# Kernel tuning notes

Measured on AMD Instinct MI355X. Metric: run time of the kernel, lower is better.

## Reference

```python
import jax, jax.numpy as jnp
import numpy as np

B, S, E, H, V = 64, 400, 512, 512, 32000


def setup_inputs() -> dict:
    key = jax.random.key(0)
    ks = jax.random.split(key, 16)
    sc = lambda fan: 1.0 / np.sqrt(fan)
    u = lambda k, shape, fan: jax.random.uniform(k, shape, jnp.float32, -sc(fan), sc(fan))
    mask = jax.random.randint(ks[3], (B, S), 0, 2).astype(bool)
    mask = mask.at[:, 0].set(True)  # ensure at least one valid position per row
    return {
        "decoder_input": jax.random.normal(ks[0], (B, E), jnp.float32),
        "previous_hidden_state": jax.random.normal(ks[1], (B, H), jnp.float32),
        "encoder_output": jax.random.normal(ks[2], (B, S, 2 * H), jnp.float32),
        "mask": mask,
        # GRUCell params (torch layout: weight_ih [3H,E], weight_hh [3H,H])
        "w_ih": u(ks[4], (3 * H, E), H),
        "w_hh": u(ks[5], (3 * H, H), H),
        "b_ih": u(ks[6], (3 * H,), H),
        "b_hh": u(ks[7], (3 * H,), H),
        # Attention params
        "Wh_w": u(ks[8], (H, 2 * H), 2 * H),
        "Wh_b": u(ks[9], (H,), 2 * H),
        "Ws_w": u(ks[10], (H, H), H),
        "Ws_b": u(ks[11], (H,), H),
        "vatt_w": u(ks[12], (1, H), H),  # Linear(H,1,bias=False)
        # Output projections
        "V_w": u(ks[13], (H, 3 * H), 3 * H),
        "V_b": u(ks[13], (H,), 3 * H),
        "Vhat_w": u(ks[14], (V, H), H),
        "Vhat_b": u(ks[15], (V,), H),
    }


def reference(decoder_input, previous_hidden_state, encoder_output, mask,
              w_ih, w_hh, b_ih, b_hh, Wh_w, Wh_b, Ws_w, Ws_b, vatt_w,
              V_w, V_b, Vhat_w, Vhat_b):
    # --- GRUCell step (torch semantics) ---
    gi = decoder_input @ w_ih.T + b_ih                  # [B, 3H]
    gh = previous_hidden_state @ w_hh.T + b_hh          # [B, 3H]
    i_r, i_z, i_n = jnp.split(gi, 3, axis=-1)
    h_r, h_z, h_n = jnp.split(gh, 3, axis=-1)
    r = jax.nn.sigmoid(i_r + h_r)
    z = jax.nn.sigmoid(i_z + h_z)
    n = jnp.tanh(i_n + r * h_n)
    hidden = (1.0 - z) * n + z * previous_hidden_state  # [B, H]

    # --- Additive (Bahdanau) attention ---
    feat = jnp.tanh(encoder_output @ Wh_w.T + Wh_b
                    + (hidden @ Ws_w.T + Ws_b)[:, None, :])   # [B, S, H]
    scores = jnp.einsum('bsh,h->bs', feat, vatt_w[0])          # [B, S]
    scores = jnp.where(mask, scores, -jnp.inf)
    attn_dist = jax.nn.softmax(scores, axis=-1)                # [B, S]

    # --- Context + output projection ---
    context_vector = jnp.einsum('bs,bsd->bd', attn_dist, encoder_output)  # [B, 2H]
    out = jnp.concatenate([hidden, context_vector], axis=-1) @ V_w.T + V_b  # [B, H]
    logits = out @ Vhat_w.T + Vhat_b                                        # [B, V]
    vocab_dist = jax.nn.softmax(logits, axis=-1)
    return (vocab_dist, attn_dist, context_vector, hidden)
```

## Files before the change

### kernel.cpp

```cpp
#include <hip/hip_runtime.h>
#include <hip/hip_bf16.h>
#include <stdint.h>

#define DI __device__ __forceinline__

using f32x2 = __attribute__((ext_vector_type(2))) float;
using f32x4 = __attribute__((ext_vector_type(4))) float;
using s16x8 = __attribute__((ext_vector_type(8))) short;

#define BB 64
#define SS 400
#define HH 512
#define VVOC 32000
#define MTOT (BB*SS)

DI short bf16r(float f){
  __hip_bfloat16 h = __float2bfloat16(f);
  union { __hip_bfloat16 h; short s; } u; u.h = h; return u.s;
}
DI float sigm(float x){ return 1.f/(1.f + __expf(-x)); }
DI float tanhfast(float x){ x = fminf(x, 12.f); float e = __expf(2.f*x); return (e-1.f)/(e+1.f); }

DI void gload16b(const __hip_bfloat16* g, short* l){
  __builtin_amdgcn_global_load_lds(
      (const __attribute__((address_space(1))) __hip_bfloat16*)g,
      (__attribute__((address_space(3))) short*)l, 16, 0, 0);
}

DI float blkmax(float v, float* red, int t){
  #pragma unroll
  for (int o = 32; o; o >>= 1) v = fmaxf(v, __shfl_xor(v, o));
  if ((t & 63) == 0) red[t >> 6] = v;
  __syncthreads();
  v = fmaxf(fmaxf(red[0], red[1]), fmaxf(red[2], red[3]));
  __syncthreads();
  return v;
}
DI float blksum(float v, float* red, int t){
  #pragma unroll
  for (int o = 32; o; o >>= 1) v += __shfl_xor(v, o);
  if ((t & 63) == 0) red[t >> 6] = v;
  __syncthreads();
  v = red[0] + red[1] + red[2] + red[3];
  __syncthreads();
  return v;
}

DI s16x8 cvt8v(f32x4 a, f32x4 b){
  s16x8 o;
  o[0]=bf16r(a[0]); o[1]=bf16r(a[1]); o[2]=bf16r(a[2]); o[3]=bf16r(a[3]);
  o[4]=bf16r(b[0]); o[5]=bf16r(b[1]); o[6]=bf16r(b[2]); o[7]=bf16r(b[3]);
  return o;
}
DI s16x8 cvt8(const float* src){
  return cvt8v(((const f32x4*)src)[0], ((const f32x4*)src)[1]);
}

DI s16x8 fragload16(const short* tile, int rbase, int kk, int l){
  int r = rbase + (l & 15);
  int c = (kk >> 3) + (l >> 4);
  int slot = c ^ (r & 7);
  return *(const s16x8*)(tile + r*64 + slot*8);
}

DI void mfma_small_body(const float* __restrict__ A, const float* __restrict__ W,
                        float* __restrict__ P, int K, int N, int c0, int kseg,
                        short* lsa, short* lsb, int t)
{
  const int kbeg = kseg*64;
  const int l = t & 63, w = t >> 6;
  #pragma unroll
  for (int q = 0; q < 2; ++q) {
    int it = q*256 + t;
    int r = it >> 3, c = it & 7;
    int slot = (c ^ (r & 7)) << 3;
    *(s16x8*)(lsa + r*64 + slot) = cvt8(A + (size_t)r*K + kbeg + c*8);
    *(s16x8*)(lsb + r*64 + slot) = cvt8(W + (size_t)(c0 + r)*K + kbeg + c*8);
  }
  __syncthreads();
  f32x4 acc[4];
  #pragma unroll
  for (int m = 0; m < 4; ++m) { f32x4 z = {0.f,0.f,0.f,0.f}; acc[m] = z; }
  #pragma unroll
  for (int kk = 0; kk < 64; kk += 32) {
    s16x8 bf = fragload16(lsb, w*16, kk, l);
    #pragma unroll
    for (int m = 0; m < 4; ++m) {
      s16x8 af = fragload16(lsa, m*16, kk, l);
      acc[m] = __builtin_amdgcn_mfma_f32_16x16x32_bf16(af, bf, acc[m], 0, 0, 0);
    }
  }
  const int kq = l >> 4, lc = l & 15;
  const int col = c0 + w*16 + lc;
  size_t pbase = (size_t)kseg * 64 * N;
  #pragma unroll
  for (int m = 0; m < 4; ++m)
    #pragma unroll
    for (int j = 0; j < 4; ++j)
      P[pbase + (size_t)(m*16 + kq*4 + j)*N + col] = acc[m][j];
}

__global__ __launch_bounds__(256) void k_pre(
    const float* __restrict__ wh, short* __restrict__ wh16,
    const unsigned int* __restrict__ mask, int mwords, int* __restrict__ flags,
    const float* __restrict__ x, const float* __restrict__ hprev,
    const float* __restrict__ w_ih, const float* __restrict__ w_hh,
    float* __restrict__ GI, float* __restrict__ GH)
{
  __shared__ __align__(16) short ls[2][64*64];
  int b = blockIdx.x, t = threadIdx.x;
  if (b < 256) {
    int i = b*256 + t;
    ((s16x8*)wh16)[i] = cvt8(wh + (size_t)i*8);
  } else if (b < 264) {
    __shared__ int f;
    if (t == 0) f = 0;
    __syncthreads();
    int loc = 0;
    for (int i = (b-256)*256 + t; i < mwords; i += 8*256) loc |= (mask[i] > 1u) ? 1 : 0;
    if (loc) atomicOr(&f, 1);
    __syncthreads();
    if (t == 0) flags[b-256] = f;
  } else {
    int gb = b - 264;
    int colI = gb % 24;
    int kseg = (gb / 24) % 8;
    int z    = gb / 192;
    mfma_small_body(z ? hprev : x, z ? w_hh : w_ih, z ? GH : GI,
                    512, 1536, colI*64, kseg, ls[0], ls[1], t);
  }
}

__global__ void gru_gate(const float* __restrict__ GI, const float* __restrict__ GH,
                         const float* __restrict__ b_ih, const float* __restrict__ b_hh,
                         const float* __restrict__ hprev, float* __restrict__ hid,
                         float* __restrict__ concat)
{
  int i = blockIdx.x*256 + threadIdx.x;
  int b = i >> 9, h = i & 511;
  float ir=0, iz=0, inn=0, hr=0, hz=0, hn=0;
  #pragma unroll
  for (int s = 0; s < 8; ++s) {
    const float* gi = GI + (size_t)s*(64*1536) + b*1536;
    const float* gh = GH + (size_t)s*(64*1536) + b*1536;
    ir += gi[h];      iz += gi[512+h];  inn += gi[1024+h];
    hr += gh[h];      hz += gh[512+h];  hn  += gh[1024+h];
  }
  ir += b_ih[h]; iz += b_ih[512+h]; inn += b_ih[1024+h];
  hr += b_hh[h]; hz += b_hh[512+h]; hn  += b_hh[1024+h];
  float r = sigm(ir + hr), z = sigm(iz + hz);
  float n = tanhfast(inn + r*hn);
  float hv = (1.f - z)*n + z*hprev[i];
  hid[i] = hv;
  concat[b*1536 + h] = hv;
}

__global__ __launch_bounds__(256) void mfma_small(
    const float* __restrict__ A, const float* __restrict__ W,
    float* __restrict__ P, int K, int N)
{
  __shared__ __align__(16) short ls[2][64*64];
  mfma_small_body(A, W, P, K, N, blockIdx.x*64, blockIdx.y, ls[0], ls[1], threadIdx.x);
}

__global__ void combineN(const float* __restrict__ P, const float* __restrict__ b1,
                         const float* __restrict__ b2, float* __restrict__ dstv,
                         int N, int total, int nseg)
{
  int i = blockIdx.x*256 + threadIdx.x;
  if (i >= total) return;
  float a = 0.f;
  for (int s = 0; s < nseg; ++s) a += P[(size_t)s*total + i];
  int c = i % N;
  if (b1) a += b1[c];
  if (b2) a += b2[c];
  dstv[i] = a;
}

__global__ __launch_bounds__(512, 2) void score_gemm_bf16(
    const float* __restrict__ A, const __hip_bfloat16* __restrict__ Bw,
    const float* __restrict__ qv, const float* __restrict__ vb, float* __restrict__ dst)
{
  __shared__ __align__(16) short lsa[128*64];
  __shared__ __align__(16) short lsb[2][512*64];
  const int t = threadIdx.x;
  const int l = t & 63;
  const int w = t >> 6;
  const int wm = w >> 2;
  const int wn = w & 3;
  const int phys = blockIdx.x;
  const int logical = (phys & 7)*25 + (phys >> 3);
  const int mrow = logical * 128;

  f32x4 par[2][2];
  #define A_LOAD(k0)                                                              \
    _Pragma("unroll")                                                             \
    for (int q = 0; q < 2; ++q) {                                                 \
      int ci = q*512 + t; int r = ci >> 3, c = ci & 7;                            \
      const f32x4* ap = (const f32x4*)(A + (size_t)(mrow + r)*1024 + (k0) + c*8); \
      par[q][0] = ap[0]; par[q][1] = ap[1];                                       \
    }
  #define A_WRITE()                                                               \
    _Pragma("unroll")                                                             \
    for (int q = 0; q < 2; ++q) {                                                 \
      int ci = q*512 + t; int r = ci >> 3, c = ci & 7;                            \
      *(s16x8*)(lsa + r*64 + ((c ^ (r & 7)) << 3)) = cvt8v(par[q][0], par[q][1]); \
    }
  #define B_STAGE(buf, k0)                                                        \
    _Pragma("unroll")                                                             \
    for (int i = 0; i < 8; ++i) {                                                 \
      int ci = i*512 + t; int r = ci >> 3, slot = ci & 7;                         \
      int c = slot ^ (r & 7);                                                     \
      gload16b(Bw + (size_t)r*1024 + (k0) + c*8, lsb[buf] + ci*8);                \
    }

  f32x4 acc[4][8];
  #pragma unroll
  for (int m = 0; m < 4; ++m)
    #pragma unroll
    for (int n = 0; n < 8; ++n) { f32x4 z = {0.f,0.f,0.f,0.f}; acc[m][n] = z; }

  A_LOAD(0)
  A_WRITE()
  B_STAGE(0, 0)
  __syncthreads();

  int cur = 0;
  for (int k = 0; k < 16; ++k) {
    if (k < 15) {
      A_LOAD((k+1)*64)
      B_STAGE(cur ^ 1, (k+1)*64)
    }
    #pragma unroll
    for (int kk = 0; kk < 64; kk += 32) {
      s16x8 bf[8];
      #pragma unroll
      for (int n = 0; n < 8; ++n) bf[n] = fragload16(lsb[cur], wn*128 + n*16, kk, l);
      #pragma unroll
      for (int m = 0; m < 4; ++m) {
        s16x8 af = fragload16(lsa, wm*64 + m*16, kk, l);
        #pragma unroll
        for (int n = 0; n < 8; ++n)
          acc[m][n] = __builtin_amdgcn_mfma_f32_16x16x32_bf16(af, bf[n], acc[m][n], 0, 0, 0);
      }
    }
    __syncthreads();
    if (k < 15) A_WRITE()
    __syncthreads();
    cur ^= 1;
  }
  #undef A_LOAD
  #undef A_WRITE
  #undef B_STAGE

  const int kq = l >> 4, lc = l & 15;
  float vv[8];
  #pragma unroll
  for (int n = 0; n < 8; ++n) vv[n] = vb[wn*128 + n*16 + lc];
  float* red = (float*)lsa;
  #pragma unroll
  for (int m = 0; m < 4; ++m) {
    #pragma unroll
    for (int j = 0; j < 4; ++j) {
      int rl = wm*64 + m*16 + kq*4 + j;
      int r = mrow + rl;
      int b = r / SS;
      const float* qb = qv + b*HH + wn*128 + lc;
      float ps = 0.f;
      #pragma unroll
      for (int n = 0; n < 8; ++n) ps += vv[n]*tanhfast(acc[m][n][j] + qb[n*16]);
      #pragma unroll
      for (int o = 1; o < 16; o <<= 1) ps += __shfl_xor(ps, o);
      if (lc == 0) red[rl*4 + wn] = ps;
    }
  }
  __syncthreads();
  if (t < 128) {
    float s = red[t*4] + red[t*4+1] + red[t*4+2] + red[t*4+3];
    dst[mrow + t] = s;
  }
}

__global__ __launch_bounds__(256) void vocab_gemm(
    const float* __restrict__ OUTm, const float* __restrict__ Vhat,
    const float* __restrict__ Vb, float* __restrict__ logits,
    float* __restrict__ MAXP, float* __restrict__ SUMP)
{
  __shared__ __align__(16) short lsa[64*64];
  __shared__ __align__(16) short lsb[64*64];
  __shared__ float red[64][8];
  const int t = threadIdx.x, l = t & 63, w = t >> 6;
  const int vrow0 = blockIdx.x * 64;

  f32x4 acc[4];
  #pragma unroll
  for (int m = 0; m < 4; ++m) { f32x4 z = {0.f,0.f,0.f,0.f}; acc[m] = z; }

  f32x4 pa0[2][2], pb0[2][2], pa1[2][2], pb1[2][2];

  #define VLOAD(pa, pb, k0)                                                     \
    _Pragma("unroll")                                                           \
    for (int q = 0; q < 2; ++q) {                                               \
      int it = q*256 + t; int r = it >> 3, c = it & 7;                          \
      const f32x4* ap = (const f32x4*)(OUTm + (size_t)r*512 + (k0) + c*8);      \
      pa[q][0] = ap[0]; pa[q][1] = ap[1];                                       \
      const f32x4* bp = (const f32x4*)(Vhat + (size_t)(vrow0 + r)*512 + (k0) + c*8); \
      pb[q][0] = bp[0]; pb[q][1] = bp[1];                                       \
    }
  #define VSTEP(pa, pb)                                                         \
    _Pragma("unroll")                                                           \
    for (int q = 0; q < 2; ++q) {                                               \
      int it = q*256 + t; int r = it >> 3, c = it & 7;                          \
      int slot = (c ^ (r & 7)) << 3;                                            \
      *(s16x8*)(lsa + r*64 + slot) = cvt8v(pa[q][0], pa[q][1]);                 \
      *(s16x8*)(lsb + r*64 + slot) = cvt8v(pb[q][0], pb[q][1]);                 \
    }                                                                           \
    __syncthreads();                                                            \
    _Pragma("unroll")                                                           \
    for (int kk = 0; kk < 64; kk += 32) {                                       \
      s16x8 bf = fragload16(lsb, w*16, kk, l);                                  \
      _Pragma("unroll")                                                         \
      for (int m = 0; m < 4; ++m) {                                             \
        s16x8 af = fragload16(lsa, m*16, kk, l);                                \
        acc[m] = __builtin_amdgcn_mfma_f32_16x16x32_bf16(af, bf, acc[m], 0,0,0);\
      }                                                                         \
    }                                                                           \
    __syncthreads();

  VLOAD(pa0, pb0, 0)
  #pragma unroll
  for (int s2 = 0; s2 < 4; ++s2) {
    int k0 = s2*128;
    if (k0 + 64 < 512) { VLOAD(pa1, pb1, k0 + 64) }
    VSTEP(pa0, pb0)
    if (k0 + 128 < 512) { VLOAD(pa0, pb0, k0 + 128) }
    VSTEP(pa1, pb1)
  }
  #undef VLOAD
  #undef VSTEP

  const int kq = l >> 4, lc = l & 15;
  const int voc = vrow0 + w*16 + lc;
  const float bias = Vb[voc];
  #pragma unroll
  for (int m = 0; m < 4; ++m)
    #pragma unroll
    for (int j = 0; j < 4; ++j) {
      acc[m][j] += bias;
      logits[(size_t)(m*16 + kq*4 + j)*VVOC + voc] = acc[m][j];
    }
  #pragma unroll
  for (int m = 0; m < 4; ++m)
    #pragma unroll
    for (int j = 0; j < 4; ++j) {
      float v = acc[m][j];
      #pragma unroll
      for (int o = 1; o < 16; o <<= 1) v = fmaxf(v, __shfl_xor(v, o));
      if (lc == 0) red[m*16 + kq*4 + j][w] = v;
    }
  __syncthreads();
  float gmax[4][4];
  #pragma unroll
  for (int m = 0; m < 4; ++m)
    #pragma unroll
    for (int j = 0; j < 4; ++j) {
      int row = m*16 + kq*4 + j;
      gmax[m][j] = fmaxf(fmaxf(red[row][0], red[row][1]), fmaxf(red[row][2], red[row][3]));
    }
  __syncthreads();
  #pragma unroll
  for (int m = 0; m < 4; ++m)
    #pragma unroll
    for (int j = 0; j < 4; ++j) {
      float s = __expf(acc[m][j] - gmax[m][j]);
      #pragma unroll
      for (int o = 1; o < 16; o <<= 1) s += __shfl_xor(s, o);
      if (lc == 0) red[m*16 + kq*4 + j][4 + w] = s;
    }
  __syncthreads();
  if (t < 64) {
    float M = fmaxf(fmaxf(red[t][0], red[t][1]), fmaxf(red[t][2], red[t][3]));
    float S = red[t][4] + red[t][5] + red[t][6] + red[t][7];
    MAXP[blockIdx.x*64 + t] = M;
    SUMP[blockIdx.x*64 + t] = S;
  }
}

__global__ __launch_bounds__(256) void vnorm(
    const float* __restrict__ MAXP, const float* __restrict__ SUMP,
    float* __restrict__ logits)
{
  __shared__ float red[4];
  int b = blockIdx.x, q = blockIdx.y, t = threadIdx.x;
  float m = -INFINITY;
  for (int i = t; i < 500; i += 256) m = fmaxf(m, MAXP[i*64 + b]);
  m = blkmax(m, red, t);
  float z = 0.f;
  for (int i = t; i < 500; i += 256) z += SUMP[i*64 + b] * __expf(MAXP[i*64 + b] - m);
  z = blksum(z, red, t);
  float inv = 1.f / z;
  f32x4* p = (f32x4*)(logits + (size_t)b*VVOC + q*8000);
  for (int i = t; i < 2000; i += 256) {
    f32x4 v = p[i];
    #pragma unroll
    for (int c = 0; c < 4; ++c) v[c] = __expf(v[c] - m) * inv;
    p[i] = v;
  }
}

__global__ void softmax_s(const float* __restrict__ score, const void* __restrict__ mask,
                          const int* __restrict__ flags, float* __restrict__ attn)
{
  __shared__ float red[4];
  int b = blockIdx.x, t = threadIdx.x;
  bool isbyte = (flags[0]|flags[1]|flags[2]|flags[3]|flags[4]|flags[5]|flags[6]|flags[7]) != 0;
  float sc0, sc1 = -INFINITY;
  {
    bool mv = isbyte ? (((const unsigned char*)mask)[b*SS + t] != 0)
                     : (((const int*)mask)[b*SS + t] != 0);
    sc0 = mv ? score[b*SS + t] : -INFINITY;
  }
  int s1 = t + 256;
  if (s1 < SS) {
    bool mv = isbyte ? (((const unsigned char*)mask)[b*SS + s1] != 0)
                     : (((const int*)mask)[b*SS + s1] != 0);
    sc1 = mv ? score[b*SS + s1] : -INFINITY;
  }
  float mx = blkmax(fmaxf(sc0, sc1), red, t);
  float e0 = __expf(sc0 - mx), e1 = __expf(sc1 - mx);
  float sum = blksum(e0 + e1, red, t);
  float inv = 1.f / sum;
  attn[b*SS + t] = e0 * inv;
  if (s1 < SS) attn[b*SS + s1] = e1 * inv;
}

__global__ void ctx_part(const float* __restrict__ attn, const float* __restrict__ enc,
                         float* __restrict__ CTXP)
{
  int b = blockIdx.x, dh = blockIdx.y, sq = blockIdx.z;
  int d0 = dh*512 + threadIdx.x*2;
  const float* a = attn + b*SS + sq*50;
  const float* e = enc + (size_t)(b*SS + sq*50)*1024 + d0;
  float lo = 0.f, hi = 0.f;
  #pragma unroll 5
  for (int s = 0; s < 50; ++s) {
    f32x2 u = *(const f32x2*)(e + (size_t)s*1024);
    float av = a[s];
    lo += av * u[0];
    hi += av * u[1];
  }
  float* dst = CTXP + (size_t)sq*65536 + b*1024 + d0;
  dst[0] = lo; dst[1] = hi;
}

__global__ void ctx_combine(const float* __restrict__ CTXP, float* __restrict__ ctx,
                            float* __restrict__ concat)
{
  int b = blockIdx.x;
  for (int d = threadIdx.x; d < 1024; d += 256) {
    float s = 0.f;
    #pragma unroll
    for (int q = 0; q < 8; ++q) s += CTXP[q*65536 + b*1024 + d];
    ctx[b*1024 + d] = s;
    concat[b*1536 + 512 + d] = s;
  }
}

extern "C" void kernel_launch(void* const* d_in, const int* in_sizes, int n_in,
                              void* d_out, int out_size, void* d_ws, size_t ws_size,
                              hipStream_t stream) {
  (void)in_sizes; (void)n_in; (void)out_size; (void)ws_size;
  const float* x      = (const float*)d_in[0];
  const float* hprev  = (const float*)d_in[1];
  const float* enc    = (const float*)d_in[2];
  const void*  mask   = d_in[3];
  const float* w_ih   = (const float*)d_in[4];
  const float* w_hh   = (const float*)d_in[5];
  const float* b_ih   = (const float*)d_in[6];
  const float* b_hh   = (const float*)d_in[7];
  const float* Wh_w   = (const float*)d_in[8];
  const float* Wh_b   = (const float*)d_in[9];
  const float* Ws_w   = (const float*)d_in[10];
  const float* Ws_b   = (const float*)d_in[11];
  const float* vatt   = (const float*)d_in[12];
  const float* V_w    = (const float*)d_in[13];
  const float* V_b    = (const float*)d_in[14];
  const float* Vhat_w = (const float*)d_in[15];
  const float* Vhat_b = (const float*)d_in[16];

  float* out   = (float*)d_out;
  float* vocab = out;
  float* attn  = out + 2048000;
  float* ctx   = out + 2073600;
  float* hid   = out + 2139136;

  float* WS     = (float*)d_ws;
  int*   FLAGS  = (int*)d_ws;
  float* GI     = WS + 16;
  float* GH     = GI + 786432;
  float* QP     = GH + 786432;
  float* Q      = QP + 262144;
  float* OUT    = Q + 32768;
  float* SCORE  = OUT + 32768;
  float* MAXP   = SCORE + 25600;
  float* SUMP   = MAXP + 32000;
  float* CTXP   = SUMP + 32000;
  float* OUTP   = CTXP + 524288;
  float* CONCAT = OUTP + 786432;
  float* ENDF   = CONCAT + 98304;
  size_t f32_bytes = ((size_t)((char*)ENDF - (char*)d_ws) + 15) & ~(size_t)15;
  short* WH16  = (short*)((char*)d_ws + f32_bytes);

  k_pre<<<dim3(648), 256, 0, stream>>>(Wh_w, WH16, (const unsigned int*)mask, 6400, FLAGS,
                                       x, hprev, w_ih, w_hh, GI, GH);
  gru_gate<<<dim3(128), 256, 0, stream>>>(GI, GH, b_ih, b_hh, hprev, hid, CONCAT);
  mfma_small<<<dim3(8, 8), 256, 0, stream>>>(hid, Ws_w, QP, 512, 512);
  combineN<<<dim3(128), 256, 0, stream>>>(QP, Ws_b, Wh_b, Q, 512, 32768, 8);
  score_gemm_bf16<<<dim3(200), 512, 0, stream>>>(
      enc, (const __hip_bfloat16*)WH16, Q, vatt, SCORE);
  softmax_s<<<dim3(64), 256, 0, stream>>>(SCORE, mask, FLAGS, attn);
  ctx_part<<<dim3(64, 2, 8), 256, 0, stream>>>(attn, enc, CTXP);
  ctx_combine<<<dim3(64), 256, 0, stream>>>(CTXP, ctx, CONCAT);
  mfma_small<<<dim3(8, 24), 256, 0, stream>>>(CONCAT, V_w, OUTP, 1536, 512);
  combineN<<<dim3(128), 256, 0, stream>>>(OUTP, V_b, nullptr, OUT, 512, 32768, 24);
  vocab_gemm<<<dim3(500), 256, 0, stream>>>(OUT, Vhat_w, Vhat_b, vocab, MAXP, SUMP);
  vnorm<<<dim3(64, 4), 256, 0, stream>>>(MAXP, SUMP, vocab);
}
```

Baseline: 136.0 us.

## Fuse GRU gate and hidden-state query projection into one kernel

Replaces the GRU gate kernel, the split-K MFMA projection of the hidden state through Ws_w, and its combine kernel with a single per-batch-row kernel. It computes the hidden state into shared memory, then does an FP32 dot product against Ws_w per output column, adding both biases. This removes two launches and the partial-sum buffer round trip. In exchange it uses only 64 blocks, and each block rereads the full Ws_w matrix with poorly coalesced per-thread row access instead of using MFMA.

```diff
diff --git a/kernel.cpp b/kernel.cpp
--- a/kernel.cpp
+++ b/kernel.cpp
@@ -131,28 +131,45 @@
   }
 }
 
-__global__ void gru_gate(const float* __restrict__ GI, const float* __restrict__ GH,
-                         const float* __restrict__ b_ih, const float* __restrict__ b_hh,
-                         const float* __restrict__ hprev, float* __restrict__ hid,
-                         float* __restrict__ concat)
-{
-  int i = blockIdx.x*256 + threadIdx.x;
-  int b = i >> 9, h = i & 511;
-  float ir=0, iz=0, inn=0, hr=0, hz=0, hn=0;
-  #pragma unroll
-  for (int s = 0; s < 8; ++s) {
-    const float* gi = GI + (size_t)s*(64*1536) + b*1536;
-    const float* gh = GH + (size_t)s*(64*1536) + b*1536;
-    ir += gi[h];      iz += gi[512+h];  inn += gi[1024+h];
-    hr += gh[h];      hz += gh[512+h];  hn  += gh[1024+h];
-  }
-  ir += b_ih[h]; iz += b_ih[512+h]; inn += b_ih[1024+h];
-  hr += b_hh[h]; hz += b_hh[512+h]; hn  += b_hh[1024+h];
-  float r = sigm(ir + hr), z = sigm(iz + hz);
-  float n = tanhfast(inn + r*hn);
-  float hv = (1.f - z)*n + z*hprev[i];
-  hid[i] = hv;
-  concat[b*1536 + h] = hv;
+__global__ __launch_bounds__(256) void fused_hidq(
+    const float* __restrict__ GI, const float* __restrict__ GH,
+    const float* __restrict__ b_ih, const float* __restrict__ b_hh,
+    const float* __restrict__ hprev, const float* __restrict__ Ws_w,
+    const float* __restrict__ Ws_b, const float* __restrict__ Wh_b,
+    float* __restrict__ hid, float* __restrict__ concat, float* __restrict__ Q)
+{
+  __shared__ float sh[512];
+  int b = blockIdx.x, t = threadIdx.x;
+  for (int h = t; h < 512; h += 256) {
+    float ir=0, iz=0, inn=0, hr=0, hz=0, hn=0;
+    #pragma unroll
+    for (int s = 0; s < 8; ++s) {
+      const float* gi = GI + (size_t)s*(64*1536) + b*1536;
+      const float* gh = GH + (size_t)s*(64*1536) + b*1536;
+      ir += gi[h];      iz += gi[512+h];  inn += gi[1024+h];
+      hr += gh[h];      hz += gh[512+h];  hn  += gh[1024+h];
+    }
+    ir += b_ih[h]; iz += b_ih[512+h]; inn += b_ih[1024+h];
+    hr += b_hh[h]; hz += b_hh[512+h]; hn  += b_hh[1024+h];
+    float r = sigm(ir + hr), z = sigm(iz + hz);
+    float n = tanhfast(inn + r*hn);
+    float hv = (1.f - z)*n + z*hprev[b*512 + h];
+    hid[b*512 + h] = hv;
+    concat[b*1536 + h] = hv;
+    sh[h] = hv;
+  }
+  __syncthreads();
+  for (int c = t; c < 512; c += 256) {
+    const f32x4* wrow = (const f32x4*)(Ws_w + (size_t)c*512);
+    float a0=0.f, a1=0.f, a2=0.f, a3=0.f;
+    #pragma unroll 8
+    for (int k4 = 0; k4 < 128; ++k4) {
+      f32x4 wv = wrow[k4];
+      f32x4 hv = *(const f32x4*)(sh + k4*4);
+      a0 += wv[0]*hv[0]; a1 += wv[1]*hv[1]; a2 += wv[2]*hv[2]; a3 += wv[3]*hv[3];
+    }
+    Q[b*512 + c] = (a0+a1)+(a2+a3) + Ws_b[c] + Wh_b[c];
+  }
 }
 
 __global__ __launch_bounds__(256) void mfma_small(
@@ -164,16 +181,13 @@
 }
 
 __global__ void combineN(const float* __restrict__ P, const float* __restrict__ b1,
-                         const float* __restrict__ b2, float* __restrict__ dstv,
-                         int N, int total, int nseg)
+                         float* __restrict__ dstv, int N, int total, int nseg)
 {
   int i = blockIdx.x*256 + threadIdx.x;
   if (i >= total) return;
   float a = 0.f;
   for (int s = 0; s < nseg; ++s) a += P[(size_t)s*total + i];
-  int c = i % N;
-  if (b1) a += b1[c];
-  if (b2) a += b2[c];
+  if (b1) a += b1[i % N];
   dstv[i] = a;
 }
 
@@ -498,8 +512,7 @@
   int*   FLAGS  = (int*)d_ws;
   float* GI     = WS + 16;
   float* GH     = GI + 786432;
-  float* QP     = GH + 786432;
-  float* Q      = QP + 262144;
+  float* Q      = GH + 786432;
   float* OUT    = Q + 32768;
   float* SCORE  = OUT + 32768;
   float* MAXP   = SCORE + 25600;
@@ -513,16 +526,15 @@
 
   k_pre<<<dim3(648), 256, 0, stream>>>(Wh_w, WH16, (const unsigned int*)mask, 6400, FLAGS,
                                        x, hprev, w_ih, w_hh, GI, GH);
-  gru_gate<<<dim3(128), 256, 0, stream>>>(GI, GH, b_ih, b_hh, hprev, hid, CONCAT);
-  mfma_small<<<dim3(8, 8), 256, 0, stream>>>(hid, Ws_w, QP, 512, 512);
-  combineN<<<dim3(128), 256, 0, stream>>>(QP, Ws_b, Wh_b, Q, 512, 32768, 8);
+  fused_hidq<<<dim3(64), 256, 0, stream>>>(GI, GH, b_ih, b_hh, hprev,
+                                           Ws_w, Ws_b, Wh_b, hid, CONCAT, Q);
   score_gemm_bf16<<<dim3(200), 512, 0, stream>>>(
       enc, (const __hip_bfloat16*)WH16, Q, vatt, SCORE);
   softmax_s<<<dim3(64), 256, 0, stream>>>(SCORE, mask, FLAGS, attn);
   ctx_part<<<dim3(64, 2, 8), 256, 0, stream>>>(attn, enc, CTXP);
   ctx_combine<<<dim3(64), 256, 0, stream>>>(CTXP, ctx, CONCAT);
   mfma_small<<<dim3(8, 24), 256, 0, stream>>>(CONCAT, V_w, OUTP, 1536, 512);
-  combineN<<<dim3(128), 256, 0, stream>>>(OUTP, V_b, nullptr, OUT, 512, 32768, 24);
+  combineN<<<dim3(128), 256, 0, stream>>>(OUTP, V_b, OUT, 512, 32768, 24);
   vocab_gemm<<<dim3(500), 256, 0, stream>>>(OUT, Vhat_w, Vhat_b, vocab, MAXP, SUMP);
   vnorm<<<dim3(64, 4), 256, 0, stream>>>(MAXP, SUMP, vocab);
 }
```

New measurement: 159.4 us. 1.17x slower.
